# Performance work log

Hardware: AMD Instinct MI355X
Metric: run time of the kernel (lower is better)

## Reference

```python
import jax, jax.numpy as jnp
import numpy as np

N_NODES = 40000            # num nodes (maybe_num_nodes)
E = 2_560_000              # input edges
SENTINEL = N_NODES * N_NODES  # key for masked-out edges; sorts last; fits int32 (1.6e9 < 2^31)


def setup_inputs() -> dict:
    key = jax.random.key(0)
    k1, k2 = jax.random.split(key)
    edge_index = jax.random.randint(k1, (2, E), 0, N_NODES, dtype=jnp.int32)
    edge_attr = jax.random.uniform(k2, (E,), dtype=jnp.float32)
    t = jnp.full((1,), 0.5, dtype=jnp.float32)  # learnable threshold parameter
    return {"edge_index": edge_index, "edge_attr": edge_attr, "t": t}


def reference(edge_index, edge_attr, t):
    """Threshold mask -> symmetrize -> coalesce (sort by (row,col), sum duplicates).

    JAX has static shapes, so compaction is expressed as masking: dropped edges get
    key=SENTINEL (sorts last) and attr contribution 0. Returns padded outputs of
    fixed size 2E plus the count of valid (unique, kept) edges. Invalid slots have
    edge_index == -1 and edge_attr == 0.
    """
    row, col = edge_index[0], edge_index[1]
    mask = edge_attr <= t[0]                      # [E] bool
    # symmetrize: stack (row,col) and (col,row), duplicate attrs  -> [2E]
    r2 = jnp.concatenate([row, col])
    c2 = jnp.concatenate([col, row])
    a2 = jnp.concatenate([edge_attr, edge_attr])
    m2 = jnp.concatenate([mask, mask])
    # coalesce: linearize key = row*N + col, sort, segment-sum duplicates
    key = jnp.where(m2, r2 * N_NODES + c2, SENTINEL)   # [2E] int32
    order = jnp.argsort(key)
    key_s = key[order]
    a_s = jnp.where(m2, a2, 0.0)[order]
    E2 = key_s.shape[0]
    new_seg = jnp.concatenate([jnp.ones((1,), bool), key_s[1:] != key_s[:-1]])
    seg = jnp.cumsum(new_seg.astype(jnp.int32)) - 1    # segment id per sorted edge
    vals = jax.ops.segment_sum(a_s, seg, num_segments=E2, indices_are_sorted=True)
    uk = jnp.full((E2,), SENTINEL, dtype=key_s.dtype).at[seg].set(key_s)
    valid = uk < SENTINEL
    out_row = jnp.where(valid, uk // N_NODES, -1)
    out_col = jnp.where(valid, uk % N_NODES, -1)
    edge_index_out = jnp.stack([out_row, out_col])     # [2, 2E] padded with -1
    edge_attr_out = jnp.where(valid, vals, 0.0)        # [2E]   padded with 0
    num_edges = jnp.sum(valid.astype(jnp.int32))
    return edge_index_out, edge_attr_out, num_edges
```

## Files before the change

### kernel.cpp

```cpp
#include <hip/hip_runtime.h>
#include <stdint.h>

#define NN 40000
#define E_IN 2560000
#define E2 5120000
#define NFINE 2500
#define NSB 20
#define SB_SHIFT 11
#define FINES_PER_SB 128
#define P2_TILES 66
#define SBCAP (P2_TILES*2048)
#define CAPB 1280
#define CSTR 16
#define P1_BLOCKS 625
#define P1_THREADS 1024

typedef unsigned long long ull;

__global__ void k_init(int* __restrict__ sbCursor, int* __restrict__ fineCursor) {
    int tid = threadIdx.x;
    for (int f = tid; f < NFINE; f += 256) fineCursor[f * CSTR] = f * CAPB;
    if (tid < NSB) sbCursor[tid * CSTR] = tid * SBCAP;
}

__global__ void __launch_bounds__(P1_THREADS) k_part1(const int* __restrict__ ei,
                                                      const float* __restrict__ ea,
                                                      const float* __restrict__ t,
                                                      int* __restrict__ sbCursor,
                                                      ull* __restrict__ pairs1) {
    __shared__ ull staged[8192];
    __shared__ int cntO[NSB * 8];
    __shared__ int off[NSB + 1], wb[NSB * 8], gbase[NSB];
    int tid = threadIdx.x;
    int oct = (tid >> 3) & 7;
    if (tid < NSB * 8) cntO[tid] = 0;
    __syncthreads();
    float t0 = t[0];
    int i0 = blockIdx.x * 4096 + tid * 4;

    float4 a4 = *(const float4*)(ea + i0);
    int4 r4 = *(const int4*)(ei + i0);
    int4 c4 = *(const int4*)(ei + E_IN + i0);
    float av[4] = {a4.x, a4.y, a4.z, a4.w};
    int rv[4] = {r4.x, r4.y, r4.z, r4.w};
    int cv[4] = {c4.x, c4.y, c4.z, c4.w};

    ull eA[4], eB[4];
    int rkA[4], rkB[4];
    bool keep[4];
#pragma unroll
    for (int k = 0; k < 4; k++) {
        keep[k] = (av[k] <= t0);
        if (keep[k]) {
            unsigned ab = __float_as_uint(av[k]);
            eA[k] = ((ull)(unsigned)rv[k] << 48) | ((ull)(unsigned)cv[k] << 32) | ab;
            eB[k] = ((ull)(unsigned)cv[k] << 48) | ((ull)(unsigned)rv[k] << 32) | ab;
            rkA[k] = atomicAdd(&cntO[((rv[k] >> SB_SHIFT) << 3) | oct], 1);
            rkB[k] = atomicAdd(&cntO[((cv[k] >> SB_SHIFT) << 3) | oct], 1);
        }
    }
    __syncthreads();
    if (tid < NSB) {
        int s = tid;
        int c[8], tot = 0;
#pragma unroll
        for (int o = 0; o < 8; o++) { c[o] = cntO[s * 8 + o]; tot += c[o]; }
        int incl = tot;
#pragma unroll
        for (int d = 1; d < 32; d <<= 1) {
            int y = __shfl_up(incl, d, 64);
            if (s >= d) incl += y;
        }
        int o0 = incl - tot;
        off[s] = o0;
        if (s == NSB - 1) off[NSB] = incl;
        int acc = o0;
#pragma unroll
        for (int o = 0; o < 8; o++) { wb[s * 8 + o] = acc; acc += c[o]; }
        gbase[s] = atomicAdd(&sbCursor[s * CSTR], tot);
    }
    __syncthreads();
#pragma unroll
    for (int k = 0; k < 4; k++) {
        if (keep[k]) {
            staged[wb[(((int)(eA[k] >> 59)) << 3) | oct] + rkA[k]] = eA[k];
            staged[wb[(((int)(eB[k] >> 59)) << 3) | oct] + rkB[k]] = eB[k];
        }
    }
    __syncthreads();
    int total = off[NSB];
    for (int i = tid; i < total; i += P1_THREADS) {
        ull e = staged[i];
        int sb = (int)(e >> 59);
        pairs1[gbase[sb] + (i - off[sb])] = e;
    }
}

__global__ void __launch_bounds__(256) k_part2(const int* __restrict__ sbCursor,
                                               int* __restrict__ fineCursor,
                                               const ull* __restrict__ pairs1,
                                               ull* __restrict__ pairs2) {
    int sb = blockIdx.x / P2_TILES;
    int tile = blockIdx.x % P2_TILES;
    int regionBase = sb * SBCAP;
    int len = sbCursor[sb * CSTR] - regionBase;
    if (len > SBCAP) len = SBCAP;
    int start = tile * 2048;
    if (start >= len) return;
    int cntT = len - start; if (cntT > 2048) cntT = 2048;
    const ull* src = pairs1 + regionBase + start;

    int fineFirst = sb * FINES_PER_SB;
    int nF = NFINE - fineFirst; if (nF > FINES_PER_SB) nF = FINES_PER_SB;

    __shared__ ull staged[2048];
    __shared__ int cnt[FINES_PER_SB], off[FINES_PER_SB + 1], gbase[FINES_PER_SB];
    int tid = threadIdx.x;
    if (tid < FINES_PER_SB) { cnt[tid] = 0; gbase[tid] = 0; }
    __syncthreads();

    ull e[8];
    int rk[8];
#pragma unroll
    for (int k = 0; k < 8; k++) {
        int i = tid + k * 256;
        if (i < cntT) {
            e[k] = src[i];
            rk[k] = atomicAdd(&cnt[(int)(e[k] >> 52) & 127], 1);
        }
    }
    __syncthreads();
    if (tid == 0) {
        int acc = 0;
        for (int s = 0; s < FINES_PER_SB; s++) { off[s] = acc; acc += cnt[s]; }
        off[FINES_PER_SB] = acc;
    }
    __syncthreads();
    if (tid < nF) gbase[tid] = atomicAdd(&fineCursor[(fineFirst + tid) * CSTR], cnt[tid]);
#pragma unroll
    for (int k = 0; k < 8; k++) {
        int i = tid + k * 256;
        if (i < cntT) staged[off[(int)(e[k] >> 52) & 127] + rk[k]] = e[k];
    }
    __syncthreads();
    int total = off[FINES_PER_SB];
    for (int i = tid; i < total; i += 256) {
        ull v = staged[i];
        int lb = (int)(v >> 52) & 127;
        pairs2[gbase[lb] + (i - off[lb])] = v;
    }
}

__device__ __forceinline__ void ce(ull& a, ull& b) {
    ull mn = a < b ? a : b;
    ull mx = a < b ? b : a;
    a = mn; b = mx;
}
__device__ __forceinline__ void sort8(ull* v) {
    ce(v[0],v[1]); ce(v[2],v[3]); ce(v[4],v[5]); ce(v[6],v[7]);
    ce(v[0],v[2]); ce(v[1],v[3]); ce(v[4],v[6]); ce(v[5],v[7]);
    ce(v[1],v[2]); ce(v[5],v[6]);
    ce(v[0],v[4]); ce(v[1],v[5]); ce(v[2],v[6]); ce(v[3],v[7]);
    ce(v[2],v[4]); ce(v[3],v[5]);
    ce(v[1],v[2]); ce(v[3],v[4]); ce(v[5],v[6]);
}
__device__ __forceinline__ void sort16(ull* v) {
    sort8(v); sort8(v + 8);
    ce(v[0],v[8]);  ce(v[1],v[9]);  ce(v[2],v[10]); ce(v[3],v[11]);
    ce(v[4],v[12]); ce(v[5],v[13]); ce(v[6],v[14]); ce(v[7],v[15]);
    ce(v[4],v[8]);  ce(v[5],v[9]);  ce(v[6],v[10]); ce(v[7],v[11]);
    ce(v[2],v[4]);  ce(v[3],v[5]);  ce(v[6],v[8]);  ce(v[7],v[9]);  ce(v[10],v[12]); ce(v[11],v[13]);
    ce(v[1],v[2]);  ce(v[3],v[4]);  ce(v[5],v[6]);  ce(v[7],v[8]);  ce(v[9],v[10]);  ce(v[11],v[12]); ce(v[13],v[14]);
}

__global__ void __launch_bounds__(512) k_sortrows(const int* __restrict__ fineCursor,
                                                  ull* __restrict__ pairs2,
                                                  int* __restrict__ uniqueCount) {
    int b = blockIdx.x;
    int base = b * CAPB;
    int n = fineCursor[b * CSTR] - base;
    if (n > CAPB) n = CAPB;
    __shared__ ull d[CAPB];
    __shared__ int cnt[512], off[512], wsum[8], ucnt[16], ubase[16];
    int tid = threadIdx.x;
    int lane = tid & 63;
    cnt[tid] = 0;
    __syncthreads();

    ull e[3]; int rk[3], sbk[3];
#pragma unroll
    for (int k = 0; k < 3; k++) {
        int i = tid + k * 512;
        if (i < n) {
            e[k] = pairs2[base + i];
            sbk[k] = (int)(e[k] >> 43) & 511;
            rk[k] = atomicAdd(&cnt[sbk[k]], 1);
        }
    }
    __syncthreads();

    int x = cnt[tid];
    int incl = x;
#pragma unroll
    for (int dlt = 1; dlt < 64; dlt <<= 1) {
        int y = __shfl_up(incl, dlt, 64);
        if (lane >= dlt) incl += y;
    }
    if (lane == 63) wsum[tid >> 6] = incl;
    __syncthreads();
    if (tid == 0) {
        int a = 0;
        for (int w = 0; w < 8; w++) { int tt = wsum[w]; wsum[w] = a; a += tt; }
    }
    __syncthreads();
    off[tid] = wsum[tid >> 6] + incl - x;
    __syncthreads();

#pragma unroll
    for (int k = 0; k < 3; k++) {
        int i = tid + k * 512;
        if (i < n) d[off[sbk[k]] + rk[k]] = e[k];
    }
    __syncthreads();

    int cn = cnt[tid]; if (cn > 16) cn = 16;
    int o0 = off[tid];
    ull v[16];
    bool big = __any(cn > 8);
    if (!big) {
#pragma unroll
        for (int k = 0; k < 8; k++) v[k] = (k < cn) ? d[o0 + k] : ~0ull;
        sort8(v);
    } else {
#pragma unroll
        for (int k = 0; k < 16; k++) v[k] = (k < cn) ? d[o0 + k] : ~0ull;
        sort16(v);
    }

    int uc = (cn > 0) ? 1 : 0;
#pragma unroll
    for (int k = 1; k < 16; k++)
        if (k < cn && (unsigned)(v[k] >> 32) != (unsigned)(v[k - 1] >> 32)) uc++;

    int uincl = uc;
#pragma unroll
    for (int dlt = 1; dlt < 64; dlt <<= 1) {
        int y = __shfl_up(uincl, dlt, 64);
        if (lane >= dlt) uincl += y;
    }
    int rowTot0 = __shfl(uincl, 31, 64);
    int rr = tid >> 5;
    int rowOff = uincl - uc - ((lane >= 32) ? rowTot0 : 0);
    if (lane == 31) ucnt[rr] = uincl;
    if (lane == 63) ucnt[rr] = uincl - rowTot0;
    __syncthreads();
    if (tid == 0) {
        int acc = 0;
        for (int s = 0; s < 16; s++) { ubase[s] = acc; acc += ucnt[s]; }
        uniqueCount[b] = acc;
    }
    __syncthreads();

    if (cn > 0) {
        ull* dst = pairs2 + base + ubase[rr] + rowOff;
        unsigned curKey = (unsigned)(v[0] >> 32);
        float curSum = __uint_as_float((unsigned)v[0]);
        int em = 0;
#pragma unroll
        for (int k = 1; k < 16; k++) {
            if (k < cn) {
                unsigned key = (unsigned)(v[k] >> 32);
                float a = __uint_as_float((unsigned)v[k]);
                if (key == curKey) {
                    curSum += a;
                } else {
                    dst[em] = ((ull)curKey << 32) | __float_as_uint(curSum);
                    em++;
                    curKey = key; curSum = a;
                }
            }
        }
        dst[em] = ((ull)curKey << 32) | __float_as_uint(curSum);
    }
}

__global__ void __launch_bounds__(1024) k_scan(const int* __restrict__ in, int n,
                                               int* __restrict__ outExcl,
                                               float* __restrict__ totalDst) {
    __shared__ int wsum[16];
    int tid = threadIdx.x, lane = tid & 63, w = tid >> 6;
    int start = tid * 3;
    int v[3], sum = 0;
#pragma unroll
    for (int k = 0; k < 3; k++) {
        int i = start + k;
        int x = (i < n) ? in[i] : 0;
        v[k] = sum;
        sum += x;
    }
    int incl = sum;
#pragma unroll
    for (int d = 1; d < 64; d <<= 1) {
        int y = __shfl_up(incl, d, 64);
        if (lane >= d) incl += y;
    }
    if (lane == 63) wsum[w] = incl;
    __syncthreads();
    if (tid < 16) {
        int x2 = wsum[tid];
        int incl2 = x2;
#pragma unroll
        for (int d = 1; d < 16; d <<= 1) {
            int y = __shfl_up(incl2, d, 64);
            if (tid >= d) incl2 += y;
        }
        wsum[tid] = incl2 - x2;
    }
    __syncthreads();
    int base = wsum[w] + incl - sum;
#pragma unroll
    for (int k = 0; k < 3; k++) {
        int i = start + k;
        if (i < n) outExcl[i] = base + v[k];
    }
    if (tid == 1023) {
        int tot = base + sum;
        outExcl[n] = tot;
        if (totalDst) totalDst[0] = (float)tot;
    }
}

__global__ void __launch_bounds__(256) k_outfill(const int* __restrict__ outBase,
                                                 const ull* __restrict__ pairs2,
                                                 float* __restrict__ out) {
    __shared__ int sOB[NFINE + 1];
    int tid = threadIdx.x;
    for (int i = tid; i <= NFINE; i += 256) sOB[i] = outBase[i];
    __syncthreads();
    int j0 = (blockIdx.x * 256 + tid) * 4;
    int T = sOB[NFINE];
    float rr[4], cc[4], aa[4];
    int lo = 0;
    if (j0 < T) {
        int hi = NFINE;
        while (hi - lo > 1) {
            int mid = (lo + hi) >> 1;
            if (sOB[mid] <= j0) lo = mid; else hi = mid;
        }
    }
#pragma unroll
    for (int k = 0; k < 4; k++) {
        int j = j0 + k;
        if (j < T) {
            while (lo < NFINE - 1 && sOB[lo + 1] <= j) lo++;
            ull e = pairs2[lo * CAPB + (j - sOB[lo])];
            rr[k] = (float)(int)(e >> 48);
            cc[k] = (float)(int)((e >> 32) & 0xFFFF);
            aa[k] = __uint_as_float((unsigned)(e & 0xFFFFFFFFu));
        } else { rr[k] = -1.0f; cc[k] = -1.0f; aa[k] = 0.0f; }
    }
    *(float4*)(out + j0)          = make_float4(rr[0], rr[1], rr[2], rr[3]);
    *(float4*)(out + E2 + j0)     = make_float4(cc[0], cc[1], cc[2], cc[3]);
    *(float4*)(out + 2 * E2 + j0) = make_float4(aa[0], aa[1], aa[2], aa[3]);
}

extern "C" void kernel_launch(void* const* d_in, const int* in_sizes, int n_in,
                              void* d_out, int out_size, void* d_ws, size_t ws_size,
                              hipStream_t stream) {
    const int*   ei = (const int*)d_in[0];
    const float* ea = (const float*)d_in[1];
    const float* t  = (const float*)d_in[2];
    float* out = (float*)d_out;

    int* sbCursor    = (int*)d_ws;
    int* fineCursor  = sbCursor + NSB * CSTR;
    int* uniqueCount = fineCursor + NFINE * CSTR;
    int* outBase     = uniqueCount + NFINE;
    ull* pairs2 = (ull*)(((uintptr_t)(outBase + NFINE + 1) + 15) & ~(uintptr_t)15);

    ull* pairs1 = (ull*)d_out;

    k_init<<<1, 256, 0, stream>>>(sbCursor, fineCursor);
    k_part1<<<P1_BLOCKS, P1_THREADS, 0, stream>>>(ei, ea, t, sbCursor, pairs1);
    k_part2<<<NSB * P2_TILES, 256, 0, stream>>>(sbCursor, fineCursor, pairs1, pairs2);
    k_sortrows<<<NFINE, 512, 0, stream>>>(fineCursor, pairs2, uniqueCount);
    k_scan<<<1, 1024, 0, stream>>>(uniqueCount, NFINE, outBase, out + (size_t)3 * E2);
    k_outfill<<<E2 / 1024, 256, 0, stream>>>(outBase, pairs2, out);
}
```

Baseline: 166.2 us.

## Enlarge part2 tiles to 1024 threads, parallel-scan offsets, grid-stride outfill

Measured after the change: 157.2 us. -5.5%, faster.

```diff
diff --git a/kernel.cpp b/kernel.cpp
--- a/kernel.cpp
+++ b/kernel.cpp
@@ -8,12 +8,14 @@
 #define NSB 20
 #define SB_SHIFT 11
 #define FINES_PER_SB 128
-#define P2_TILES 66
-#define SBCAP (P2_TILES*2048)
+#define P2_TILES 17
+#define P2_TILE 8192
+#define SBCAP 135168
 #define CAPB 1280
 #define CSTR 16
 #define P1_BLOCKS 625
 #define P1_THREADS 1024
+#define OF_BLOCKS 1250
 
 typedef unsigned long long ull;
 
@@ -96,25 +98,25 @@
     }
 }
 
-__global__ void __launch_bounds__(256) k_part2(const int* __restrict__ sbCursor,
-                                               int* __restrict__ fineCursor,
-                                               const ull* __restrict__ pairs1,
-                                               ull* __restrict__ pairs2) {
+__global__ void __launch_bounds__(1024) k_part2(const int* __restrict__ sbCursor,
+                                                int* __restrict__ fineCursor,
+                                                const ull* __restrict__ pairs1,
+                                                ull* __restrict__ pairs2) {
     int sb = blockIdx.x / P2_TILES;
     int tile = blockIdx.x % P2_TILES;
     int regionBase = sb * SBCAP;
     int len = sbCursor[sb * CSTR] - regionBase;
     if (len > SBCAP) len = SBCAP;
-    int start = tile * 2048;
+    int start = tile * P2_TILE;
     if (start >= len) return;
-    int cntT = len - start; if (cntT > 2048) cntT = 2048;
+    int cntT = len - start; if (cntT > P2_TILE) cntT = P2_TILE;
     const ull* src = pairs1 + regionBase + start;
 
     int fineFirst = sb * FINES_PER_SB;
     int nF = NFINE - fineFirst; if (nF > FINES_PER_SB) nF = FINES_PER_SB;
 
-    __shared__ ull staged[2048];
-    __shared__ int cnt[FINES_PER_SB], off[FINES_PER_SB + 1], gbase[FINES_PER_SB];
+    __shared__ ull staged[P2_TILE];
+    __shared__ int cnt[FINES_PER_SB], off[FINES_PER_SB + 1], gbase[FINES_PER_SB], wsum2[2];
     int tid = threadIdx.x;
     if (tid < FINES_PER_SB) { cnt[tid] = 0; gbase[tid] = 0; }
     __syncthreads();
@@ -123,28 +125,42 @@
     int rk[8];
 #pragma unroll
     for (int k = 0; k < 8; k++) {
-        int i = tid + k * 256;
+        int i = tid + k * 1024;
         if (i < cntT) {
             e[k] = src[i];
             rk[k] = atomicAdd(&cnt[(int)(e[k] >> 52) & 127], 1);
         }
     }
     __syncthreads();
-    if (tid == 0) {
-        int acc = 0;
-        for (int s = 0; s < FINES_PER_SB; s++) { off[s] = acc; acc += cnt[s]; }
-        off[FINES_PER_SB] = acc;
-    }
-    __syncthreads();
-    if (tid < nF) gbase[tid] = atomicAdd(&fineCursor[(fineFirst + tid) * CSTR], cnt[tid]);
+    int x = 0, incl = 0;
+    if (tid < FINES_PER_SB) {
+        x = cnt[tid];
+        incl = x;
+        int lane = tid & 63;
+#pragma unroll
+        for (int d = 1; d < 64; d <<= 1) {
+            int y = __shfl_up(incl, d, 64);
+            if (lane >= d) incl += y;
+        }
+        if (lane == 63) wsum2[tid >> 6] = incl;
+    }
+    __syncthreads();
+    if (tid == 0) { int a = wsum2[0]; wsum2[0] = 0; wsum2[1] = a; }
+    __syncthreads();
+    if (tid < FINES_PER_SB) {
+        off[tid] = wsum2[tid >> 6] + incl - x;
+        if (tid == FINES_PER_SB - 1) off[FINES_PER_SB] = wsum2[1] + incl;
+        if (tid < nF) gbase[tid] = atomicAdd(&fineCursor[(fineFirst + tid) * CSTR], x);
+    }
+    __syncthreads();
 #pragma unroll
     for (int k = 0; k < 8; k++) {
-        int i = tid + k * 256;
+        int i = tid + k * 1024;
         if (i < cntT) staged[off[(int)(e[k] >> 52) & 127] + rk[k]] = e[k];
     }
     __syncthreads();
     int total = off[FINES_PER_SB];
-    for (int i = tid; i < total; i += 256) {
+    for (int i = tid; i < total; i += 1024) {
         ull v = staged[i];
         int lb = (int)(v >> 52) & 127;
         pairs2[gbase[lb] + (i - off[lb])] = v;
@@ -337,31 +353,33 @@
     int tid = threadIdx.x;
     for (int i = tid; i <= NFINE; i += 256) sOB[i] = outBase[i];
     __syncthreads();
-    int j0 = (blockIdx.x * 256 + tid) * 4;
     int T = sOB[NFINE];
-    float rr[4], cc[4], aa[4];
-    int lo = 0;
-    if (j0 < T) {
-        int hi = NFINE;
-        while (hi - lo > 1) {
-            int mid = (lo + hi) >> 1;
-            if (sOB[mid] <= j0) lo = mid; else hi = mid;
-        }
-    }
-#pragma unroll
-    for (int k = 0; k < 4; k++) {
-        int j = j0 + k;
-        if (j < T) {
-            while (lo < NFINE - 1 && sOB[lo + 1] <= j) lo++;
-            ull e = pairs2[lo * CAPB + (j - sOB[lo])];
-            rr[k] = (float)(int)(e >> 48);
-            cc[k] = (float)(int)((e >> 32) & 0xFFFF);
-            aa[k] = __uint_as_float((unsigned)(e & 0xFFFFFFFFu));
-        } else { rr[k] = -1.0f; cc[k] = -1.0f; aa[k] = 0.0f; }
-    }
-    *(float4*)(out + j0)          = make_float4(rr[0], rr[1], rr[2], rr[3]);
-    *(float4*)(out + E2 + j0)     = make_float4(cc[0], cc[1], cc[2], cc[3]);
-    *(float4*)(out + 2 * E2 + j0) = make_float4(aa[0], aa[1], aa[2], aa[3]);
+    for (int tile = blockIdx.x; tile < E2 / 1024; tile += OF_BLOCKS) {
+        int j0 = (tile * 256 + tid) * 4;
+        float rr[4], cc[4], aa[4];
+        int lo = 0;
+        if (j0 < T) {
+            int hi = NFINE;
+            while (hi - lo > 1) {
+                int mid = (lo + hi) >> 1;
+                if (sOB[mid] <= j0) lo = mid; else hi = mid;
+            }
+        }
+#pragma unroll
+        for (int k = 0; k < 4; k++) {
+            int j = j0 + k;
+            if (j < T) {
+                while (lo < NFINE - 1 && sOB[lo + 1] <= j) lo++;
+                ull e = pairs2[lo * CAPB + (j - sOB[lo])];
+                rr[k] = (float)(int)(e >> 48);
+                cc[k] = (float)(int)((e >> 32) & 0xFFFF);
+                aa[k] = __uint_as_float((unsigned)(e & 0xFFFFFFFFu));
+            } else { rr[k] = -1.0f; cc[k] = -1.0f; aa[k] = 0.0f; }
+        }
+        *(float4*)(out + j0)          = make_float4(rr[0], rr[1], rr[2], rr[3]);
+        *(float4*)(out + E2 + j0)     = make_float4(cc[0], cc[1], cc[2], cc[3]);
+        *(float4*)(out + 2 * E2 + j0) = make_float4(aa[0], aa[1], aa[2], aa[3]);
+    }
 }
 
 extern "C" void kernel_launch(void* const* d_in, const int* in_sizes, int n_in,
@@ -382,8 +400,8 @@
 
     k_init<<<1, 256, 0, stream>>>(sbCursor, fineCursor);
     k_part1<<<P1_BLOCKS, P1_THREADS, 0, stream>>>(ei, ea, t, sbCursor, pairs1);
-    k_part2<<<NSB * P2_TILES, 256, 0, stream>>>(sbCursor, fineCursor, pairs1, pairs2);
+    k_part2<<<NSB * P2_TILES, 1024, 0, stream>>>(sbCursor, fineCursor, pairs1, pairs2);
     k_sortrows<<<NFINE, 512, 0, stream>>>(fineCursor, pairs2, uniqueCount);
     k_scan<<<1, 1024, 0, stream>>>(uniqueCount, NFINE, outBase, out + (size_t)3 * E2);
-    k_outfill<<<E2 / 1024, 256, 0, stream>>>(outBase, pairs2, out);
-}
+    k_outfill<<<OF_BLOCKS, 256, 0, stream>>>(outBase, pairs2, out);
+}
```
